# Kernel optimization log

Hardware: AMD Instinct MI355X
Metric: run time of the kernel (lower is better)

The kernel has to match this reference:

```python
import jax, jax.numpy as jnp
import numpy as np
import math

DIM = 4096
BATCH = 8192
SCALE = 1.0 / math.sqrt(DIM)


def fwht(x):
    """Fast Walsh-Hadamard Transform along last axis (iterative butterfly).
    Faithful to the torch reshape/slice/cat implementation; the Python while
    loop is over log2(n) static stages, fine under jit.
    """
    n = x.shape[-1]
    h = 1
    while h < n:
        x = x.reshape(*x.shape[:-1], n // (2 * h), 2 * h)
        a = x[..., :h]
        b = x[..., h:]
        x = jnp.concatenate([a + b, a - b], axis=-1)
        x = x.reshape(*x.shape[:-2], n)
        h *= 2
    return x


def setup_inputs() -> dict:
    key = jax.random.key(0)
    kx, k1, k2, k3, k4 = jax.random.split(key, 5)
    x = jax.random.normal(kx, (BATCH, DIM), dtype=jnp.float32)
    # +/-1 random sign diagonals
    d1 = (jax.random.randint(k1, (DIM,), 0, 2).astype(jnp.float32) * 2 - 1)
    d2 = (jax.random.randint(k2, (DIM,), 0, 2).astype(jnp.float32) * 2 - 1)
    # |N(0,1)| gaussian diagonal
    gauss_d = jnp.abs(jax.random.normal(k3, (DIM,), dtype=jnp.float32))
    # random permutation of [0, DIM)
    perm = jax.random.permutation(k4, DIM).astype(jnp.int64)
    return {"x": x, "d1": d1, "d2": d2, "gauss_d": gauss_d, "perm": perm}


def reference(x, d1, d2, gauss_d, perm):
    # W ~= D2 @ H @ G @ Pi @ H @ D1, applied to each row of x
    y = x * d1
    y = fwht(y)
    y = y[..., perm]
    y = y * gauss_d
    y = fwht(y)
    y = y * d2
    return y * SCALE
```

## Files before the change

### kernel.cpp

```cpp
#include <hip/hip_runtime.h>
#include <math.h>

#define DIM 4096
#define FF_SCALE 0.015625f

__device__ __forceinline__ void fwht16(float v[16]) {
#pragma unroll
    for (int h = 1; h < 16; h <<= 1) {
#pragma unroll
        for (int i = 0; i < 16; ++i) {
            if ((i & h) == 0) {
                float a = v[i];
                float b = v[i + h];
                v[i] = a + b;
                v[i + h] = a - b;
            }
        }
    }
}

__device__ __forceinline__ int swz(int i) {
    return i ^ (((i >> 8) & 1) << 4);
}

__global__ __launch_bounds__(256) void fastfood_kernel(
    const float* __restrict__ x,
    const float* __restrict__ d1,
    const float* __restrict__ d2,
    const float* __restrict__ gauss_d,
    const int* __restrict__ perm,
    float* __restrict__ out)
{
    __shared__ float lds[DIM];
    const int t = threadIdx.x;
    const int row = blockIdx.x;
    const float* xrow = x + (size_t)row * DIM;
    float* orow = out + (size_t)row * DIM;

    float v[16];

    {
        const float4* xv = (const float4*)(xrow + t * 16);
        const float4* dv = (const float4*)(d1 + t * 16);
#pragma unroll
        for (int q = 0; q < 4; ++q) {
            float4 aa = xv[q];
            float4 dd = dv[q];
            v[4 * q + 0] = aa.x * dd.x;
            v[4 * q + 1] = aa.y * dd.y;
            v[4 * q + 2] = aa.z * dd.z;
            v[4 * q + 3] = aa.w * dd.w;
        }
    }
    fwht16(v);
    {
        int g = t ^ ((t >> 4) & 1);
        float4* l = (float4*)(lds + g * 16);
#pragma unroll
        for (int q = 0; q < 4; ++q)
            l[q] = make_float4(v[4 * q + 0], v[4 * q + 1], v[4 * q + 2], v[4 * q + 3]);
    }
    __syncthreads();

    {
        const int a = t >> 4, c = t & 15;
        const int base = a * 256 + c;
        const int xb = (a & 1) << 4;
#pragma unroll
        for (int b = 0; b < 16; ++b)
            v[b] = lds[(base + b * 16) ^ xb];
        fwht16(v);
#pragma unroll
        for (int b = 0; b < 16; ++b)
            lds[(base + b * 16) ^ xb] = v[b];
    }
    __syncthreads();

    {
#pragma unroll
        for (int a = 0; a < 16; ++a)
            v[a] = lds[(a * 256 + t) ^ ((a & 1) << 4)];
        fwht16(v);
#pragma unroll
        for (int a = 0; a < 16; ++a)
            lds[(a * 256 + t) ^ ((a & 1) << 4)] = v[a];
    }
    __syncthreads();

    {
        const int4* pv = (const int4*)(perm + t * 16);
        const float4* gv = (const float4*)(gauss_d + t * 16);
        int pidx[16];
        float g[16];
#pragma unroll
        for (int q = 0; q < 4; ++q) {
            int4 pp = pv[q];
            float4 gg = gv[q];
            pidx[4 * q + 0] = pp.x; pidx[4 * q + 1] = pp.y;
            pidx[4 * q + 2] = pp.z; pidx[4 * q + 3] = pp.w;
            g[4 * q + 0] = gg.x; g[4 * q + 1] = gg.y;
            g[4 * q + 2] = gg.z; g[4 * q + 3] = gg.w;
        }
#pragma unroll
        for (int k = 0; k < 16; ++k) {
            int pi = pidx[k];
            v[k] = lds[swz(pi)] * g[k];
        }
    }
    fwht16(v);
    __syncthreads();
    {
        int g = t ^ ((t >> 4) & 1);
        float4* l = (float4*)(lds + g * 16);
#pragma unroll
        for (int q = 0; q < 4; ++q)
            l[q] = make_float4(v[4 * q + 0], v[4 * q + 1], v[4 * q + 2], v[4 * q + 3]);
    }
    __syncthreads();

    {
        const int a = t >> 4, c = t & 15;
        const int base = a * 256 + c;
        const int xb = (a & 1) << 4;
#pragma unroll
        for (int b = 0; b < 16; ++b)
            v[b] = lds[(base + b * 16) ^ xb];
        fwht16(v);
#pragma unroll
        for (int b = 0; b < 16; ++b)
            lds[(base + b * 16) ^ xb] = v[b];
    }
    __syncthreads();

    {
#pragma unroll
        for (int a = 0; a < 16; ++a)
            v[a] = lds[(a * 256 + t) ^ ((a & 1) << 4)];
        fwht16(v);
#pragma unroll
        for (int a = 0; a < 16; ++a) {
            int i = a * 256 + t;
            orow[i] = v[a] * d2[i] * FF_SCALE;
        }
    }
}

extern "C" void kernel_launch(void* const* d_in, const int* in_sizes, int n_in,
                              void* d_out, int out_size, void* d_ws, size_t ws_size,
                              hipStream_t stream) {
    const float* x       = (const float*)d_in[0];
    const float* d1      = (const float*)d_in[1];
    const float* d2      = (const float*)d_in[2];
    const float* gauss_d = (const float*)d_in[3];
    const int*   perm    = (const int*)d_in[4];
    float* out = (float*)d_out;

    const int batch = in_sizes[0] / DIM;
    fastfood_kernel<<<batch, 256, 0, stream>>>(x, d1, d2, gauss_d, perm, out);
}
```

Baseline: 249.4 us.

## Replace LDS transpose stages with DPP quad butterflies and XOR-swizzled layout

Each FWHT now runs two 16-point stages in registers plus two extra radix-2 stages across lanes in a quad using DPP moves. This cuts each transform from three LDS round trips to two and drops several barriers per row. A new XOR swizzle on LDS addresses is meant to avoid bank conflicts for the new access patterns. The scale is folded into gauss_d. The trade-off is extra VALU work for the DPP butterflies, and the output store pattern changes to 64-float strides per thread.

```diff
diff --git a/kernel.cpp b/kernel.cpp
--- a/kernel.cpp
+++ b/kernel.cpp
@@ -1,8 +1,11 @@
 #include <hip/hip_runtime.h>
-#include <math.h>
 
 #define DIM 4096
 #define FF_SCALE 0.015625f
+
+__device__ __forceinline__ int phys(int i) {
+    return i ^ ((((i >> 5) ^ (i >> 8) ^ (i >> 11)) & 7) << 2);
+}
 
 __device__ __forceinline__ void fwht16(float v[16]) {
 #pragma unroll
@@ -10,8 +13,7 @@
 #pragma unroll
         for (int i = 0; i < 16; ++i) {
             if ((i & h) == 0) {
-                float a = v[i];
-                float b = v[i + h];
+                float a = v[i], b = v[i + h];
                 v[i] = a + b;
                 v[i + h] = a - b;
             }
@@ -19,8 +21,19 @@
     }
 }
 
-__device__ __forceinline__ int swz(int i) {
-    return i ^ (((i >> 8) & 1) << 4);
+template <int CTRL>
+__device__ __forceinline__ float qperm(float x) {
+    return __int_as_float(
+        __builtin_amdgcn_mov_dpp(__float_as_int(x), CTRL, 0xF, 0xF, true));
+}
+
+template <int CTRL>
+__device__ __forceinline__ void qbutterfly(float v[16], float s) {
+#pragma unroll
+    for (int e = 0; e < 16; ++e) {
+        float p = qperm<CTRL>(v[e]);
+        v[e] = fmaf(v[e], s, p);
+    }
 }
 
 __global__ __launch_bounds__(256) void fastfood_kernel(
@@ -33,115 +46,79 @@
 {
     __shared__ float lds[DIM];
     const int t = threadIdx.x;
-    const int row = blockIdx.x;
-    const float* xrow = x + (size_t)row * DIM;
-    float* orow = out + (size_t)row * DIM;
+    const float s1 = (t & 1) ? -1.f : 1.f;
+    const float s2 = (t & 2) ? -1.f : 1.f;
+    const int B = (t >> 2) + ((t & 3) << 10);
+    const size_t rowoff = (size_t)blockIdx.x * DIM;
 
     float v[16];
 
     {
-        const float4* xv = (const float4*)(xrow + t * 16);
+        const float4* xv = (const float4*)(x + rowoff + t * 16);
         const float4* dv = (const float4*)(d1 + t * 16);
 #pragma unroll
         for (int q = 0; q < 4; ++q) {
-            float4 aa = xv[q];
-            float4 dd = dv[q];
-            v[4 * q + 0] = aa.x * dd.x;
-            v[4 * q + 1] = aa.y * dd.y;
-            v[4 * q + 2] = aa.z * dd.z;
-            v[4 * q + 3] = aa.w * dd.w;
+            float4 a = xv[q], d = dv[q];
+            v[4 * q + 0] = a.x * d.x;
+            v[4 * q + 1] = a.y * d.y;
+            v[4 * q + 2] = a.z * d.z;
+            v[4 * q + 3] = a.w * d.w;
         }
     }
+
     fwht16(v);
-    {
-        int g = t ^ ((t >> 4) & 1);
-        float4* l = (float4*)(lds + g * 16);
+    qbutterfly<0xB1>(v, s1);
+    qbutterfly<0x4E>(v, s2);
+
 #pragma unroll
-        for (int q = 0; q < 4; ++q)
-            l[q] = make_float4(v[4 * q + 0], v[4 * q + 1], v[4 * q + 2], v[4 * q + 3]);
-    }
+    for (int q = 0; q < 4; ++q)
+        *(float4*)(lds + phys(t * 16 + 4 * q)) =
+            make_float4(v[4 * q], v[4 * q + 1], v[4 * q + 2], v[4 * q + 3]);
     __syncthreads();
 
-    {
-        const int a = t >> 4, c = t & 15;
-        const int base = a * 256 + c;
-        const int xb = (a & 1) << 4;
+    float w[16];
 #pragma unroll
-        for (int b = 0; b < 16; ++b)
-            v[b] = lds[(base + b * 16) ^ xb];
-        fwht16(v);
+    for (int c = 0; c < 16; ++c) w[c] = lds[phys(B + (c << 6))];
+    fwht16(w);
+    qbutterfly<0xB1>(w, s1);
+    qbutterfly<0x4E>(w, s2);
 #pragma unroll
-        for (int b = 0; b < 16; ++b)
-            lds[(base + b * 16) ^ xb] = v[b];
-    }
-    __syncthreads();
-
-    {
-#pragma unroll
-        for (int a = 0; a < 16; ++a)
-            v[a] = lds[(a * 256 + t) ^ ((a & 1) << 4)];
-        fwht16(v);
-#pragma unroll
-        for (int a = 0; a < 16; ++a)
-            lds[(a * 256 + t) ^ ((a & 1) << 4)] = v[a];
-    }
+    for (int c = 0; c < 16; ++c) lds[phys(B + (c << 6))] = w[c];
     __syncthreads();
 
     {
         const int4* pv = (const int4*)(perm + t * 16);
         const float4* gv = (const float4*)(gauss_d + t * 16);
-        int pidx[16];
-        float g[16];
 #pragma unroll
         for (int q = 0; q < 4; ++q) {
-            int4 pp = pv[q];
-            float4 gg = gv[q];
-            pidx[4 * q + 0] = pp.x; pidx[4 * q + 1] = pp.y;
-            pidx[4 * q + 2] = pp.z; pidx[4 * q + 3] = pp.w;
-            g[4 * q + 0] = gg.x; g[4 * q + 1] = gg.y;
-            g[4 * q + 2] = gg.z; g[4 * q + 3] = gg.w;
-        }
-#pragma unroll
-        for (int k = 0; k < 16; ++k) {
-            int pi = pidx[k];
-            v[k] = lds[swz(pi)] * g[k];
+            int4 p4 = pv[q];
+            float4 g4 = gv[q];
+            v[4 * q + 0] = lds[phys(p4.x)] * (g4.x * FF_SCALE);
+            v[4 * q + 1] = lds[phys(p4.y)] * (g4.y * FF_SCALE);
+            v[4 * q + 2] = lds[phys(p4.z)] * (g4.z * FF_SCALE);
+            v[4 * q + 3] = lds[phys(p4.w)] * (g4.w * FF_SCALE);
         }
     }
+
     fwht16(v);
+    qbutterfly<0xB1>(v, s1);
+    qbutterfly<0x4E>(v, s2);
     __syncthreads();
-    {
-        int g = t ^ ((t >> 4) & 1);
-        float4* l = (float4*)(lds + g * 16);
 #pragma unroll
-        for (int q = 0; q < 4; ++q)
-            l[q] = make_float4(v[4 * q + 0], v[4 * q + 1], v[4 * q + 2], v[4 * q + 3]);
-    }
+    for (int q = 0; q < 4; ++q)
+        *(float4*)(lds + phys(t * 16 + 4 * q)) =
+            make_float4(v[4 * q], v[4 * q + 1], v[4 * q + 2], v[4 * q + 3]);
     __syncthreads();
 
-    {
-        const int a = t >> 4, c = t & 15;
-        const int base = a * 256 + c;
-        const int xb = (a & 1) << 4;
 #pragma unroll
-        for (int b = 0; b < 16; ++b)
-            v[b] = lds[(base + b * 16) ^ xb];
-        fwht16(v);
+    for (int c = 0; c < 16; ++c) w[c] = lds[phys(B + (c << 6))];
+    fwht16(w);
+    qbutterfly<0xB1>(w, s1);
+    qbutterfly<0x4E>(w, s2);
 #pragma unroll
-        for (int b = 0; b < 16; ++b)
-            lds[(base + b * 16) ^ xb] = v[b];
-    }
-    __syncthreads();
-
-    {
-#pragma unroll
-        for (int a = 0; a < 16; ++a)
-            v[a] = lds[(a * 256 + t) ^ ((a & 1) << 4)];
-        fwht16(v);
-#pragma unroll
-        for (int a = 0; a < 16; ++a) {
-            int i = a * 256 + t;
-            orow[i] = v[a] * d2[i] * FF_SCALE;
-        }
+    for (int c = 0; c < 16; ++c) {
+        int i = B + (c << 6);
+        out[rowoff + i] = w[c] * d2[i];
     }
 }
 
```

Result: slower. 257.2 us (+3.1%).
